# Kernel optimization log

Hardware: AMD Instinct MI355X
Metric: run time of the kernel (lower is better)

Reference implementation:

```python
import jax, jax.numpy as jnp
import numpy as np

B, N, C = 8, 1024, 768
H, D = 12, 64  # num_heads, head_dim
SCALE = D ** -0.5


def setup_inputs() -> dict:
    key = jax.random.key(0)
    ks = jax.random.split(key, 6)
    x = jax.random.normal(ks[0], (B, N, C), dtype=jnp.float32)
    # per-head Linear weights stacked: [H, D, C] (torch Linear stores [out, in])
    Wq = jax.random.normal(ks[1], (H, D, C), dtype=jnp.float32) * 0.02
    Wk = jax.random.normal(ks[2], (H, D, C), dtype=jnp.float32) * 0.02
    Wv = jax.random.normal(ks[3], (H, D, C), dtype=jnp.float32) * 0.02
    Wp = jax.random.normal(ks[4], (C, C), dtype=jnp.float32) * 0.02
    bp = jnp.zeros((C,), dtype=jnp.float32)
    return {"x": x, "Wq": Wq, "Wk": Wk, "Wv": Wv, "Wp": Wp, "bp": bp}


def reference(x, Wq, Wk, Wv, Wp, bp):
    # Per-head projections (batched across heads): [B, H, N, D]
    q = jnp.einsum('bnc,hdc->bhnd', x, Wq) * SCALE
    k = jnp.einsum('bnc,hdc->bhnd', x, Wk)
    v = jnp.einsum('bnc,hdc->bhnd', x, Wv)
    # Scaled dot-product attention per head
    attn = jax.nn.softmax(jnp.einsum('bhnd,bhmd->bhnm', q, k), axis=-1)
    out = jnp.einsum('bhnm,bhmd->bhnd', attn, v)
    # Concat heads along last dim == transpose to [B, N, H, D] then reshape
    out = out.transpose(0, 2, 1, 3).reshape(x.shape[0], x.shape[1], -1)
    # Output projection
    return out @ Wp.T + bp
```

## Files before the change

kernel.cpp:

```cpp
#include <hip/hip_runtime.h>

typedef unsigned short u16;
typedef __attribute__((ext_vector_type(8))) __bf16 bf16x8;
typedef __attribute__((ext_vector_type(4))) float f32x4;

__device__ __forceinline__ u16 f2bf(float f) {
    union { float f; unsigned u; } v; v.f = f;
    unsigned u = v.u;
    u += 0x7FFFu + ((u >> 16) & 1u);
    return (u16)(u >> 16);
}

typedef const __attribute__((address_space(1))) void GV;
typedef __attribute__((address_space(3))) void LV;
__device__ __forceinline__ void gl2lds16(const void* g, void* l) {
    __builtin_amdgcn_global_load_lds((GV*)g, (LV*)l, 16, 0, 0);
}

__global__ __launch_bounds__(256) void cast_all(
    const float* __restrict__ x,  const float* __restrict__ Wq,
    const float* __restrict__ Wk, const float* __restrict__ Wv,
    const float* __restrict__ Wp,
    u16* __restrict__ xb, u16* __restrict__ wb, u16* __restrict__ wpb)
{
    int bid = blockIdx.x;
    const float4* s; ushort4* d; int idx;
    if (bid < 6144) {
        s = (const float4*)x; d = (ushort4*)xb; idx = bid * 256 + threadIdx.x;
    } else {
        int t = bid - 6144;
        int w = t / 576;
        idx = (t - w * 576) * 256 + threadIdx.x;
        s = (const float4*)(w == 0 ? Wq : w == 1 ? Wk : w == 2 ? Wv : Wp);
        d = (ushort4*)(w == 3 ? wpb : wb + w * 589824);
    }
    float4 f = s[idx];
    ushort4 o;
    o.x = f2bf(f.x); o.y = f2bf(f.y); o.z = f2bf(f.z); o.w = f2bf(f.w);
    d[idx] = o;
}

__device__ __forceinline__ void stage_g(const u16* src, int k0, u16* lds, int g, int tid) {
    int i = g * 512 + tid;
    int row = i >> 3, p = i & 7;
    int l = p ^ (row & 7);
    gl2lds16(src + (size_t)row * 768 + k0 + l * 8, lds + i * 8);
}
__device__ __forceinline__ const bf16x8* frag64(const u16* lds, int row, int kc) {
    return reinterpret_cast<const bf16x8*>(lds + row * 64 + ((kc ^ (row & 7)) * 8));
}

__device__ __forceinline__ void kloop256(
    const u16* __restrict__ aSrc, const u16* __restrict__ bSrc,
    u16* As, u16* Bs, f32x4 (&acc)[4][4],
    int tid, int wm, int wn, int quad, int l16)
{
    #pragma unroll
    for (int tt = 0; tt < 2; tt++) {
        #pragma unroll
        for (int g = 0; g < 4; g++) stage_g(aSrc, tt * 64, As + tt * 16384, g, tid);
        #pragma unroll
        for (int g = 0; g < 2; g++) stage_g(bSrc, tt * 64, Bs + tt * 8192, g, tid);
    }
    asm volatile("s_waitcnt vmcnt(6)" ::: "memory");
    __builtin_amdgcn_s_barrier();
    asm volatile("" ::: "memory");

    int buf = 0;
    for (int t = 0; t < 12; t++) {
        const u16* Ab = As + buf * 16384;
        const u16* Bb = Bs + buf * 8192;
        int sb = buf + 2; if (sb >= 3) sb -= 3;
        u16* Asb = As + sb * 16384;
        u16* Bsb = Bs + sb * 8192;
        const bool pf = (t + 2 < 12);
        const int k2 = (t + 2) * 64;

        bf16x8 a[4], b[4];
        #pragma unroll
        for (int mi = 0; mi < 4; mi++) a[mi] = *frag64(Ab, wm * 64 + mi * 16 + l16, quad);
        #pragma unroll
        for (int ni = 0; ni < 4; ni++) b[ni] = *frag64(Bb, wn * 64 + ni * 16 + l16, quad);
        if (pf) {
            stage_g(aSrc, k2, Asb, 0, tid);
            stage_g(aSrc, k2, Asb, 1, tid);
            stage_g(aSrc, k2, Asb, 2, tid);
        }
        __builtin_amdgcn_s_barrier();
        asm volatile("" ::: "memory");
        __builtin_amdgcn_s_setprio(1);
        #pragma unroll
        for (int mi = 0; mi < 4; mi++)
            #pragma unroll
            for (int ni = 0; ni < 4; ni++)
                acc[mi][ni] = __builtin_amdgcn_mfma_f32_16x16x32_bf16(a[mi], b[ni], acc[mi][ni], 0, 0, 0);
        __builtin_amdgcn_s_setprio(0);

        #pragma unroll
        for (int mi = 0; mi < 4; mi++) a[mi] = *frag64(Ab, wm * 64 + mi * 16 + l16, 4 + quad);
        #pragma unroll
        for (int ni = 0; ni < 4; ni++) b[ni] = *frag64(Bb, wn * 64 + ni * 16 + l16, 4 + quad);
        if (pf) {
            stage_g(aSrc, k2, Asb, 3, tid);
            stage_g(bSrc, k2, Bsb, 0, tid);
            stage_g(bSrc, k2, Bsb, 1, tid);
        }
        if (t <= 9)       asm volatile("s_waitcnt vmcnt(6)" ::: "memory");
        else if (t == 10) asm volatile("s_waitcnt vmcnt(0)" ::: "memory");
        __builtin_amdgcn_s_barrier();
        asm volatile("" ::: "memory");
        __builtin_amdgcn_s_setprio(1);
        #pragma unroll
        for (int mi = 0; mi < 4; mi++)
            #pragma unroll
            for (int ni = 0; ni < 4; ni++)
                acc[mi][ni] = __builtin_amdgcn_mfma_f32_16x16x32_bf16(a[mi], b[ni], acc[mi][ni], 0, 0, 0);
        __builtin_amdgcn_s_setprio(0);

        buf++; if (buf == 3) buf = 0;
    }
}

__global__ __launch_bounds__(512, 2) void gemm_qkv(
    const u16* __restrict__ A, const u16* __restrict__ Bm,
    u16* __restrict__ qo, u16* __restrict__ ko, u16* __restrict__ vto)
{
    __shared__ u16 As[3][16384];
    __shared__ u16 Bs[3][8192];
    const int tid = threadIdx.x;
    const int wave = tid >> 6, lane = tid & 63;
    const int quad = lane >> 4, l16 = lane & 15;
    const int wm = wave >> 1, wn = wave & 1;
    const int id = blockIdx.x + 18 * blockIdx.y;
    const int nid = (id & 7) * 72 + (id >> 3);
    const int bx = nid % 18, by = nid / 18;
    const int rowBase = by * 256;
    const int colBase = bx * 128;

    f32x4 acc[4][4] = {};
    kloop256(A + (size_t)rowBase * 768, Bm + (size_t)colBase * 768,
             &As[0][0], &Bs[0][0], acc, tid, wm, wn, quad, l16);

    #pragma unroll
    for (int mi = 0; mi < 4; mi++) {
        #pragma unroll
        for (int ni = 0; ni < 4; ni++) {
            int gj = colBase + wn * 64 + ni * 16 + l16;
            int which = gj / 768;
            int r = gj - which * 768;
            int h = r >> 6, d = r & 63;
            int gi0 = rowBase + wm * 64 + mi * 16 + quad * 4;
            int b_ = gi0 >> 10;
            int n0 = gi0 & 1023;
            if (which == 2) {
                ushort4 pk;
                pk.x = f2bf(acc[mi][ni][0]);
                pk.y = f2bf(acc[mi][ni][1]);
                pk.z = f2bf(acc[mi][ni][2]);
                pk.w = f2bf(acc[mi][ni][3]);
                *reinterpret_cast<ushort4*>(vto + ((size_t)(b_ * 12 + h) * 64 + d) * 1024 + n0) = pk;
            } else {
                float s = (which == 0) ? 0.125f : 1.0f;
                u16* dst = (which == 0 ? qo : ko) + ((size_t)(b_ * 12 + h) * 1024 + n0) * 64 + d;
                #pragma unroll
                for (int rr = 0; rr < 4; rr++)
                    dst[(size_t)rr * 64] = f2bf(acc[mi][ni][rr] * s);
            }
        }
    }
}

__global__ __launch_bounds__(512, 4) void attn_fwd(
    const u16* __restrict__ q, const u16* __restrict__ k,
    const u16* __restrict__ vt, u16* __restrict__ ao)
{
    __shared__ u16 Ks[2][4096];
    __shared__ u16 Vs[2][4096];
    __shared__ u16 Ps[256][72];
    const int bh = blockIdx.x, qt = blockIdx.y;
    const int b = bh / 12, h = bh - b * 12;
    const int tid = threadIdx.x;
    const int wave = tid >> 6, lane = tid & 63;
    const int quad = lane >> 4, l16 = lane & 15;
    const int swz = l16 & 7;
    u16 (*PsW)[72] = &Ps[wave * 32];

    const u16* qb = q + (size_t)bh * 65536 + ((size_t)qt * 256 + wave * 32) * 64;
    const u16* kb = k + (size_t)bh * 65536;
    const u16* vb = vt + (size_t)bh * 65536;

    auto stage = [&](int buf, int j0) {
        int i = tid;
        int row = i >> 3, cp = i & 7;
        int cl = cp ^ (row & 7);
        gl2lds16((const char*)kb + (size_t)(j0 + row) * 128 + cl * 16,
                 (char*)&Ks[buf][0] + i * 16);
        gl2lds16((const char*)vb + (size_t)row * 2048 + (size_t)j0 * 2 + cl * 16,
                 (char*)&Vs[buf][0] + i * 16);
    };

    stage(0, 0);

    bf16x8 qf[2][2];
    #pragma unroll
    for (int ni = 0; ni < 2; ni++)
        #pragma unroll
        for (int ks = 0; ks < 2; ks++)
            qf[ni][ks] = *reinterpret_cast<const bf16x8*>(qb + (ni * 16 + l16) * 64 + ks * 32 + quad * 8);

    f32x4 o[2][4] = {};
    float lsum[2] = {0.f, 0.f};

    __syncthreads();

    int buf = 0;
    for (int j0 = 0; j0 < 1024; j0 += 64) {
        if (j0 + 64 < 1024) stage(buf ^ 1, j0 + 64);

        f32x4 s[4][2] = {};
        #pragma unroll
        for (int ks = 0; ks < 2; ks++) {
            bf16x8 kf[4];
            #pragma unroll
            for (int mi = 0; mi < 4; mi++) {
                int row = mi * 16 + l16;
                int ch = (ks * 4 + quad) ^ swz;
                kf[mi] = *reinterpret_cast<const bf16x8*>(&Ks[buf][row * 64 + ch * 8]);
            }
            #pragma unroll
            for (int mi = 0; mi < 4; mi++)
                #pragma unroll
                for (int ni = 0; ni < 2; ni++)
                    s[mi][ni] = __builtin_amdgcn_mfma_f32_16x16x32_bf16(kf[mi], qf[ni][ks], s[mi][ni], 0, 0, 0);
        }

        #pragma unroll
        for (int mi = 0; mi < 4; mi++) {
            #pragma unroll
            for (int ni = 0; ni < 2; ni++) {
                float p0 = __expf(s[mi][ni][0]);
                float p1 = __expf(s[mi][ni][1]);
                float p2 = __expf(s[mi][ni][2]);
                float p3 = __expf(s[mi][ni][3]);
                lsum[ni] += (p0 + p1) + (p2 + p3);
                ushort4 pk;
                pk.x = f2bf(p0); pk.y = f2bf(p1); pk.z = f2bf(p2); pk.w = f2bf(p3);
                *reinterpret_cast<ushort4*>(&PsW[ni * 16 + l16][mi * 16 + quad * 4]) = pk;
            }
        }

        #pragma unroll
        for (int ks = 0; ks < 2; ks++) {
            bf16x8 vf[4], pf[2];
            #pragma unroll
            for (int di = 0; di < 4; di++) {
                int row = di * 16 + l16;
                int ch = (ks * 4 + quad) ^ swz;
                vf[di] = *reinterpret_cast<const bf16x8*>(&Vs[buf][row * 64 + ch * 8]);
            }
            #pragma unroll
            for (int mi = 0; mi < 2; mi++)
                pf[mi] = *reinterpret_cast<const bf16x8*>(&PsW[mi * 16 + l16][ks * 32 + quad * 8]);
            #pragma unroll
            for (int mi = 0; mi < 2; mi++)
                #pragma unroll
                for (int di = 0; di < 4; di++)
                    o[mi][di] = __builtin_amdgcn_mfma_f32_16x16x32_bf16(pf[mi], vf[di], o[mi][di], 0, 0, 0);
        }

        __syncthreads();
        buf ^= 1;
    }

    #pragma unroll
    for (int ni = 0; ni < 2; ni++) {
        lsum[ni] += __shfl_xor(lsum[ni], 16, 64);
        lsum[ni] += __shfl_xor(lsum[ni], 32, 64);
    }

    #pragma unroll
    for (int mi = 0; mi < 2; mi++) {
        #pragma unroll
        for (int r = 0; r < 4; r++) {
            float lv = __shfl(lsum[mi], quad * 4 + r, 16);
            float inv = 1.0f / lv;
            int n = qt * 256 + wave * 32 + mi * 16 + quad * 4 + r;
            size_t base = (size_t)(b * 1024 + n) * 768 + h * 64;
            #pragma unroll
            for (int di = 0; di < 4; di++)
                ao[base + di * 16 + l16] = f2bf(o[mi][di][r] * inv);
        }
    }
}

__global__ __launch_bounds__(512, 2) void gemm_proj(
    const u16* __restrict__ A, const u16* __restrict__ Bm,
    const float* __restrict__ bias, float* __restrict__ out)
{
    __shared__ u16 As[3][16384];
    __shared__ u16 Bs[3][8192];
    const int tid = threadIdx.x;
    const int wave = tid >> 6, lane = tid & 63;
    const int quad = lane >> 4, l16 = lane & 15;
    const int wm = wave >> 1, wn = wave & 1;
    const int id = blockIdx.x + 6 * blockIdx.y;
    const int nid = (id & 7) * 24 + (id >> 3);
    const int bx = nid % 6, by = nid / 6;
    const int rowBase = by * 256;
    const int colBase = bx * 128;

    f32x4 acc[4][4] = {};
    kloop256(A + (size_t)rowBase * 768, Bm + (size_t)colBase * 768,
             &As[0][0], &Bs[0][0], acc, tid, wm, wn, quad, l16);

    #pragma unroll
    for (int mi = 0; mi < 4; mi++) {
        #pragma unroll
        for (int ni = 0; ni < 4; ni++) {
            int gj = colBase + wn * 64 + ni * 16 + l16;
            float bv = bias[gj];
            int gi0 = rowBase + wm * 64 + mi * 16 + quad * 4;
            #pragma unroll
            for (int rr2 = 0; rr2 < 4; rr2++)
                out[(size_t)(gi0 + rr2) * 768 + gj] = acc[mi][ni][rr2] + bv;
        }
    }
}

extern "C" void kernel_launch(void* const* d_in, const int* in_sizes, int n_in,
                              void* d_out, int out_size, void* d_ws, size_t ws_size,
                              hipStream_t stream) {
    const float* x  = (const float*)d_in[0];
    const float* Wq = (const float*)d_in[1];
    const float* Wk = (const float*)d_in[2];
    const float* Wv = (const float*)d_in[3];
    const float* Wp = (const float*)d_in[4];
    const float* bp = (const float*)d_in[5];
    float* out = (float*)d_out;

    u16* xb  = (u16*)d_ws;
    u16* wb  = xb  + 6291456;
    u16* wpb = wb  + 1769472;
    u16* qo  = wpb + 589824;
    u16* ko  = qo  + 6291456;
    u16* vto = ko  + 6291456;
    u16* ao  = vto + 6291456;

    cast_all<<<8448, 256, 0, stream>>>(x, Wq, Wk, Wv, Wp, xb, wb, wpb);
    gemm_qkv<<<dim3(18, 32), 512, 0, stream>>>(xb, wb, qo, ko, vto);
    attn_fwd<<<dim3(96, 4), 512, 0, stream>>>(qo, ko, vto, ao);
    gemm_proj<<<dim3(6, 32), 512, 0, stream>>>(ao, wpb, bp, out);
}
```

Measured before the change: 195.7 us.

## Switch attention to 32x32x16 MFMA with register-resident P via permlane32 swap

Rewrites the attention kernel to use 32x32x16 bf16 MFMAs instead of 16x16x32. The exponentiated score tile is packed into bf16 and rearranged in registers with permlane32_swap, so it feeds the PV MFMA directly without the LDS P buffer round-trip. Blocks shrink to 256 threads covering 128 queries, with twice as many blocks in the grid. This removes LDS write/read traffic and one shared buffer, but adds larger accumulator register pressure and depends on correct lane layout for the swap.

Result: faster. 189.4 us (-3.2%).

```diff
diff --git a/kernel.cpp b/kernel.cpp
--- a/kernel.cpp
+++ b/kernel.cpp
@@ -3,12 +3,23 @@
 typedef unsigned short u16;
 typedef __attribute__((ext_vector_type(8))) __bf16 bf16x8;
 typedef __attribute__((ext_vector_type(4))) float f32x4;
+typedef __attribute__((ext_vector_type(16))) float f32x16;
 
 __device__ __forceinline__ u16 f2bf(float f) {
     union { float f; unsigned u; } v; v.f = f;
     unsigned u = v.u;
     u += 0x7FFFu + ((u >> 16) & 1u);
     return (u16)(u >> 16);
+}
+
+__device__ __forceinline__ unsigned pk2(float lo, float hi) {
+    union { __bf16 h[2]; unsigned u; } x;
+    x.h[0] = (__bf16)lo; x.h[1] = (__bf16)hi;
+    return x.u;
+}
+__device__ __forceinline__ void pswap(unsigned &a, unsigned &b) {
+    auto r = __builtin_amdgcn_permlane32_swap(a, b, false, false);
+    a = r[0]; b = r[1];
 }
 
 typedef const __attribute__((address_space(1))) void GV;
@@ -170,46 +181,51 @@
     }
 }
 
-__global__ __launch_bounds__(512, 4) void attn_fwd(
+__global__ __launch_bounds__(256, 3) void attn_fwd(
     const u16* __restrict__ q, const u16* __restrict__ k,
     const u16* __restrict__ vt, u16* __restrict__ ao)
 {
     __shared__ u16 Ks[2][4096];
     __shared__ u16 Vs[2][4096];
-    __shared__ u16 Ps[256][72];
     const int bh = blockIdx.x, qt = blockIdx.y;
     const int b = bh / 12, h = bh - b * 12;
     const int tid = threadIdx.x;
     const int wave = tid >> 6, lane = tid & 63;
-    const int quad = lane >> 4, l16 = lane & 15;
-    const int swz = l16 & 7;
-    u16 (*PsW)[72] = &Ps[wave * 32];
-
-    const u16* qb = q + (size_t)bh * 65536 + ((size_t)qt * 256 + wave * 32) * 64;
+    const int l31 = lane & 31, hi = lane >> 5;
+    const int sw = l31 & 7;
+
+    const u16* qb = q + (size_t)bh * 65536 + ((size_t)qt * 128 + wave * 32) * 64;
     const u16* kb = k + (size_t)bh * 65536;
     const u16* vb = vt + (size_t)bh * 65536;
 
     auto stage = [&](int buf, int j0) {
-        int i = tid;
-        int row = i >> 3, cp = i & 7;
-        int cl = cp ^ (row & 7);
-        gl2lds16((const char*)kb + (size_t)(j0 + row) * 128 + cl * 16,
-                 (char*)&Ks[buf][0] + i * 16);
-        gl2lds16((const char*)vb + (size_t)row * 2048 + (size_t)j0 * 2 + cl * 16,
-                 (char*)&Vs[buf][0] + i * 16);
+        #pragma unroll
+        for (int r = 0; r < 2; r++) {
+            int i = r * 256 + tid;
+            int row = i >> 3, cp = i & 7;
+            int cl = cp ^ (row & 7);
+            gl2lds16((const char*)kb + (size_t)(j0 + row) * 128 + cl * 16,
+                     (char*)&Ks[buf][0] + i * 16);
+        }
+        #pragma unroll
+        for (int r = 0; r < 2; r++) {
+            int i = r * 256 + tid;
+            int row = i >> 3, cp = i & 7;
+            int cl = cp ^ (row & 7);
+            gl2lds16((const char*)vb + (size_t)row * 2048 + (size_t)j0 * 2 + cl * 16,
+                     (char*)&Vs[buf][0] + i * 16);
+        }
     };
 
     stage(0, 0);
 
-    bf16x8 qf[2][2];
-    #pragma unroll
-    for (int ni = 0; ni < 2; ni++)
-        #pragma unroll
-        for (int ks = 0; ks < 2; ks++)
-            qf[ni][ks] = *reinterpret_cast<const bf16x8*>(qb + (ni * 16 + l16) * 64 + ks * 32 + quad * 8);
-
-    f32x4 o[2][4] = {};
-    float lsum[2] = {0.f, 0.f};
+    bf16x8 qf[4];
+    #pragma unroll
+    for (int dk = 0; dk < 4; dk++)
+        qf[dk] = *reinterpret_cast<const bf16x8*>(qb + l31 * 64 + dk * 16 + hi * 8);
+
+    f32x16 o0 = {}, o1 = {};
+    float lsum = 0.f;
 
     __syncthreads();
 
@@ -217,79 +233,62 @@
     for (int j0 = 0; j0 < 1024; j0 += 64) {
         if (j0 + 64 < 1024) stage(buf ^ 1, j0 + 64);
 
-        f32x4 s[4][2] = {};
-        #pragma unroll
-        for (int ks = 0; ks < 2; ks++) {
-            bf16x8 kf[4];
+        f32x16 s0 = {}, s1 = {};
+        #pragma unroll
+        for (int dk = 0; dk < 4; dk++) {
+            int ch = ((2 * dk + hi) ^ sw) * 8;
+            bf16x8 kf0 = *reinterpret_cast<const bf16x8*>(&Ks[buf][l31 * 64 + ch]);
+            bf16x8 kf1 = *reinterpret_cast<const bf16x8*>(&Ks[buf][(32 + l31) * 64 + ch]);
+            s0 = __builtin_amdgcn_mfma_f32_32x32x16_bf16(kf0, qf[dk], s0, 0, 0, 0);
+            s1 = __builtin_amdgcn_mfma_f32_32x32x16_bf16(kf1, qf[dk], s1, 0, 0, 0);
+        }
+
+        bf16x8 pa[4];
+        #pragma unroll
+        for (int kbk = 0; kbk < 2; kbk++) {
+            float p[16];
             #pragma unroll
-            for (int mi = 0; mi < 4; mi++) {
-                int row = mi * 16 + l16;
-                int ch = (ks * 4 + quad) ^ swz;
-                kf[mi] = *reinterpret_cast<const bf16x8*>(&Ks[buf][row * 64 + ch * 8]);
+            for (int r = 0; r < 16; r++) {
+                p[r] = __expf(kbk ? s1[r] : s0[r]);
+                lsum += p[r];
             }
-            #pragma unroll
-            for (int mi = 0; mi < 4; mi++)
-                #pragma unroll
-                for (int ni = 0; ni < 2; ni++)
-                    s[mi][ni] = __builtin_amdgcn_mfma_f32_16x16x32_bf16(kf[mi], qf[ni][ks], s[mi][ni], 0, 0, 0);
-        }
-
-        #pragma unroll
-        for (int mi = 0; mi < 4; mi++) {
-            #pragma unroll
-            for (int ni = 0; ni < 2; ni++) {
-                float p0 = __expf(s[mi][ni][0]);
-                float p1 = __expf(s[mi][ni][1]);
-                float p2 = __expf(s[mi][ni][2]);
-                float p3 = __expf(s[mi][ni][3]);
-                lsum[ni] += (p0 + p1) + (p2 + p3);
-                ushort4 pk;
-                pk.x = f2bf(p0); pk.y = f2bf(p1); pk.z = f2bf(p2); pk.w = f2bf(p3);
-                *reinterpret_cast<ushort4*>(&PsW[ni * 16 + l16][mi * 16 + quad * 4]) = pk;
-            }
-        }
-
-        #pragma unroll
-        for (int ks = 0; ks < 2; ks++) {
-            bf16x8 vf[4], pf[2];
-            #pragma unroll
-            for (int di = 0; di < 4; di++) {
-                int row = di * 16 + l16;
-                int ch = (ks * 4 + quad) ^ swz;
-                vf[di] = *reinterpret_cast<const bf16x8*>(&Vs[buf][row * 64 + ch * 8]);
-            }
-            #pragma unroll
-            for (int mi = 0; mi < 2; mi++)
-                pf[mi] = *reinterpret_cast<const bf16x8*>(&PsW[mi * 16 + l16][ks * 32 + quad * 8]);
-            #pragma unroll
-            for (int mi = 0; mi < 2; mi++)
-                #pragma unroll
-                for (int di = 0; di < 4; di++)
-                    o[mi][di] = __builtin_amdgcn_mfma_f32_16x16x32_bf16(pf[mi], vf[di], o[mi][di], 0, 0, 0);
+            unsigned W00 = pk2(p[0],  p[1]),  W01 = pk2(p[2],  p[3]);
+            unsigned W10 = pk2(p[4],  p[5]),  W11 = pk2(p[6],  p[7]);
+            unsigned W20 = pk2(p[8],  p[9]),  W21 = pk2(p[10], p[11]);
+            unsigned W30 = pk2(p[12], p[13]), W31 = pk2(p[14], p[15]);
+            pswap(W00, W10); pswap(W01, W11);
+            pswap(W20, W30); pswap(W21, W31);
+            union { unsigned u[4]; bf16x8 v; } pk0, pk1;
+            pk0.u[0] = W00; pk0.u[1] = W01; pk0.u[2] = W10; pk0.u[3] = W11;
+            pk1.u[0] = W20; pk1.u[1] = W21; pk1.u[2] = W30; pk1.u[3] = W31;
+            pa[kbk * 2 + 0] = pk0.v;
+            pa[kbk * 2 + 1] = pk1.v;
+        }
+
+        #pragma unroll
+        for (int ks = 0; ks < 4; ks++) {
+            int ch = ((2 * ks + hi) ^ sw) * 8;
+            bf16x8 vf0 = *reinterpret_cast<const bf16x8*>(&Vs[buf][l31 * 64 + ch]);
+            bf16x8 vf1 = *reinterpret_cast<const bf16x8*>(&Vs[buf][(32 + l31) * 64 + ch]);
+            o0 = __builtin_amdgcn_mfma_f32_32x32x16_bf16(pa[ks], vf0, o0, 0, 0, 0);
+            o1 = __builtin_amdgcn_mfma_f32_32x32x16_bf16(pa[ks], vf1, o1, 0, 0, 0);
         }
 
         __syncthreads();
         buf ^= 1;
     }
 
-    #pragma unroll
-    for (int ni = 0; ni < 2; ni++) {
-        lsum[ni] += __shfl_xor(lsum[ni], 16, 64);
-        lsum[ni] += __shfl_xor(lsum[ni], 32, 64);
-    }
-
-    #pragma unroll
-    for (int mi = 0; mi < 2; mi++) {
-        #pragma unroll
-        for (int r = 0; r < 4; r++) {
-            float lv = __shfl(lsum[mi], quad * 4 + r, 16);
-            float inv = 1.0f / lv;
-            int n = qt * 256 + wave * 32 + mi * 16 + quad * 4 + r;
-            size_t base = (size_t)(b * 1024 + n) * 768 + h * 64;
-            #pragma unroll
-            for (int di = 0; di < 4; di++)
-                ao[base + di * 16 + l16] = f2bf(o[mi][di][r] * inv);
-        }
+    lsum += __shfl_xor(lsum, 32, 64);
+
+    #pragma unroll
+    for (int r = 0; r < 16; r++) {
+        int qrow = (r & 3) + 8 * (r >> 2) + 4 * hi;
+        float lv = __shfl(lsum, qrow, 32);
+        float inv = 1.0f / lv;
+        int n = qt * 128 + wave * 32 + qrow;
+        size_t base = (size_t)(b * 1024 + n) * 768 + h * 64;
+        ao[base + l31]      = f2bf(o0[r] * inv);
+        ao[base + 32 + l31] = f2bf(o1[r] * inv);
     }
 }
 
@@ -348,6 +347,6 @@
 
     cast_all<<<8448, 256, 0, stream>>>(x, Wq, Wk, Wv, Wp, xb, wb, wpb);
     gemm_qkv<<<dim3(18, 32), 512, 0, stream>>>(xb, wb, qo, ko, vto);
-    attn_fwd<<<dim3(96, 4), 512, 0, stream>>>(qo, ko, vto, ao);
+    attn_fwd<<<dim3(96, 8), 256, 0, stream>>>(qo, ko, vto, ao);
     gemm_proj<<<dim3(6, 32), 512, 0, stream>>>(ao, wpb, bp, out);
 }
```
